# Kernel tuning notes

Hardware: AMD Instinct MI355X
Metric: run time of the kernel (lower is better)

The kernel has to match this reference:

```python
import jax, jax.numpy as jnp
import numpy as np

N_NODES = 50000
N_EDGES = 400000
DIMS = [128, 1024, 512, 256, 64, 1]  # ConvGraphNet layer widths


def setup_inputs() -> dict:
    key = jax.random.key(0)
    ks = jax.random.split(key, 2 + 2 * 5)
    inp = {}
    inp["x"] = jax.random.normal(ks[0], (N_NODES, DIMS[0]), dtype=jnp.float32)
    inp["edge_index"] = jax.random.randint(ks[1], (2, N_EDGES), 0, N_NODES, dtype=jnp.int32)
    for i in range(5):
        fan_in, fan_out = DIMS[i], DIMS[i + 1]
        scale = (1.0 / np.sqrt(fan_in)).astype(np.float32)
        inp[f"W{i+1}"] = jax.random.normal(ks[2 + 2 * i], (fan_in, fan_out), dtype=jnp.float32) * scale
        inp[f"b{i+1}"] = jax.random.normal(ks[3 + 2 * i], (fan_out,), dtype=jnp.float32) * 0.01
    return inp


def _gcn_forward(x, edge_index, params):
    # PyG GCNConv: add self-loops, symmetric deg^{-1/2} normalization,
    # h = x @ W, out[dst] += norm * h[src], + bias. ReLU after each layer.
    src, dst = edge_index[0], edge_index[1]
    loop = jnp.arange(N_NODES, dtype=src.dtype)
    src_f = jnp.concatenate([src, loop])  # [E + N]
    dst_f = jnp.concatenate([dst, loop])
    deg = jax.ops.segment_sum(jnp.ones_like(src_f, dtype=x.dtype), dst_f, num_segments=N_NODES)
    dinv = jnp.where(deg > 0, jax.lax.rsqrt(jnp.maximum(deg, 1e-12)), 0.0).astype(x.dtype)
    norm = (dinv[src_f] * dinv[dst_f])[:, None]  # [E + N, 1]
    for W, b in params:
        h = x @ W                      # [N, F_out] dense GEMM (small)
        msg = h[src_f] * norm          # gather + scale  [E+N, F_out]
        agg = jax.ops.segment_sum(msg, dst_f, num_segments=N_NODES)  # scatter-add
        x = jax.nn.relu(agg + b)
    return x


def reference(x, edge_index, W1, b1, W2, b2, W3, b3, W4, b4, W5, b5):
    params = [(W1, b1), (W2, b2), (W3, b3), (W4, b4), (W5, b5)]
    return _gcn_forward(x, edge_index, params)
```

## Files before the change

kernel.cpp:

```cpp
#include <hip/hip_runtime.h>
#include <hip/hip_bf16.h>

#define N_NODES_DIM0 128

typedef unsigned short u16;
typedef unsigned int u32;
typedef __attribute__((ext_vector_type(8))) short short8;
typedef __attribute__((ext_vector_type(4))) float f32x4;

__device__ __forceinline__ float bf2f(u16 h) { return __uint_as_float((u32)h << 16); }
__device__ __forceinline__ u16 f2bf(float f) {
    u32 u = __float_as_uint(f);
    u32 r = (u + 0x7FFFu + ((u >> 16) & 1u)) >> 16;
    return (u16)r;
}

__device__ __forceinline__ void gl2lds16(const u16* g, u16* lds_base) {
    __builtin_amdgcn_global_load_lds(
        (const __attribute__((address_space(1))) u32*)g,
        (__attribute__((address_space(3))) u32*)lds_base, 16, 0, 0);
}


__global__ void hist_kernel(const int* __restrict__ dst, int* __restrict__ cnt, int e) {
    int i = blockIdx.x * blockDim.x + threadIdx.x;
    if (i < e) atomicAdd(&cnt[dst[i]], 1);
}

__global__ void alloc_kernel(const int* __restrict__ cnt, int* __restrict__ row_start,
                             float* __restrict__ dinv, int* __restrict__ cursor, int n) {
    int i = blockIdx.x * blockDim.x + threadIdx.x;
    int lane = threadIdx.x & 63;
    int v = (i < n) ? cnt[i] : 0;
    int s = v;
#pragma unroll
    for (int off = 1; off < 64; off <<= 1) {
        int x = __shfl_up(s, off, 64);
        if (lane >= off) s += x;
    }
    int total = __shfl(s, 63, 64);
    int base = 0;
    if (lane == 0) base = atomicAdd(cursor, total);
    base = __shfl(base, 0, 64);
    if (i < n) {
        row_start[i] = base + s - v;
        dinv[i] = rsqrtf((float)v + 1.0f);
    }
}

__global__ void fill_kernel(const int* __restrict__ src, const int* __restrict__ dst,
                            int* __restrict__ row_start, int* __restrict__ csr_src, int e) {
    int i = blockIdx.x * blockDim.x + threadIdx.x;
    if (i < e) {
        int d = dst[i];
        int pos = atomicAdd(&row_start[d], 1);
        csr_src[pos] = src[i];
    }
}

__global__ __launch_bounds__(256) void prep_kernel(
    const float* __restrict__ W0, const float* __restrict__ W1,
    const float* __restrict__ W2, const float* __restrict__ W3, u16* __restrict__ Wt,
    const float* __restrict__ x, const float* __restrict__ dinv,
    u16* __restrict__ Y, int N) {
    int bid = blockIdx.x;
    if (bid < 784) {
        __shared__ float tile[32][33];
        const float* W; u16* out; int K, F, kb, nb;
        if (bid < 128)      { W = W0; out = Wt;          K = 128;  F = 1024; kb = bid & 3;  nb = bid >> 2; }
        else if (bid < 640) { int l = bid - 128; W = W1; out = Wt + 131072; K = 1024; F = 512; kb = l & 31; nb = l >> 5; }
        else if (bid < 768) { int l = bid - 640; W = W2; out = Wt + 655360; K = 512;  F = 256; kb = l & 15; nb = l >> 4; }
        else                { int l = bid - 768; W = W3; out = Wt + 786432; K = 256;  F = 64;  kb = l & 7;  nb = l >> 3; }
        int k0 = kb * 32, n0 = nb * 32;
        int tx = threadIdx.x & 31, ty = threadIdx.x >> 5;
#pragma unroll
        for (int i = 0; i < 4; ++i) {
            int k = ty + i * 8;
            tile[k][tx] = W[(size_t)(k0 + k) * F + n0 + tx];
        }
        __syncthreads();
#pragma unroll
        for (int i = 0; i < 4; ++i) {
            int n = ty + i * 8;
            out[(size_t)(n0 + n) * K + k0 + tx] = f2bf(tile[tx][n]);
        }
    } else {
        int gid = (bid - 784) * 256 + threadIdx.x;
        int node = gid >> 5;
        int c4 = (gid & 31) * 4;
        if (node >= N) return;
        float dv = dinv[node];
        float4 v = *reinterpret_cast<const float4*>(x + (size_t)node * 128 + c4);
        ushort4 r;
        r.x = f2bf(dv * v.x); r.y = f2bf(dv * v.y);
        r.z = f2bf(dv * v.z); r.w = f2bf(dv * v.w);
        *reinterpret_cast<ushort4*>(Y + (size_t)node * 128 + c4) = r;
    }
}

__device__ __forceinline__ void add8v(float* acc, short8 v) {
#pragma unroll
    for (int w = 0; w < 8; ++w) acc[w] += bf2f((u16)v[w]);
}
__device__ __forceinline__ void add16p(float* acc, const u16* p) {
    short8 a = *reinterpret_cast<const short8*>(p);
    short8 b = *reinterpret_cast<const short8*>(p + 8);
    add8v(acc, a); add8v(acc + 8, b);
}

__device__ __forceinline__ void gather_sum16(float* acc, const u16* __restrict__ base,
                                             const int* __restrict__ csr_src,
                                             int beg, int end, int stride, int ch) {
    int e = beg;
    int nfull = (end - beg) >> 3;
    if (nfull > 0) {
        int i0 = csr_src[e],     i1 = csr_src[e + 1], i2 = csr_src[e + 2], i3 = csr_src[e + 3];
        int i4 = csr_src[e + 4], i5 = csr_src[e + 5], i6 = csr_src[e + 6], i7 = csr_src[e + 7];
        for (int b = 0; b < nfull; ++b) {
            const u16* p0 = base + (size_t)i0 * stride + ch;
            const u16* p1 = base + (size_t)i1 * stride + ch;
            const u16* p2 = base + (size_t)i2 * stride + ch;
            const u16* p3 = base + (size_t)i3 * stride + ch;
            const u16* p4 = base + (size_t)i4 * stride + ch;
            const u16* p5 = base + (size_t)i5 * stride + ch;
            const u16* p6 = base + (size_t)i6 * stride + ch;
            const u16* p7 = base + (size_t)i7 * stride + ch;
            short8 a0 = *reinterpret_cast<const short8*>(p0), b0 = *reinterpret_cast<const short8*>(p0 + 8);
            short8 a1 = *reinterpret_cast<const short8*>(p1), b1 = *reinterpret_cast<const short8*>(p1 + 8);
            short8 a2 = *reinterpret_cast<const short8*>(p2), b2 = *reinterpret_cast<const short8*>(p2 + 8);
            short8 a3 = *reinterpret_cast<const short8*>(p3), b3 = *reinterpret_cast<const short8*>(p3 + 8);
            short8 a4 = *reinterpret_cast<const short8*>(p4), b4 = *reinterpret_cast<const short8*>(p4 + 8);
            short8 a5 = *reinterpret_cast<const short8*>(p5), b5 = *reinterpret_cast<const short8*>(p5 + 8);
            short8 a6 = *reinterpret_cast<const short8*>(p6), b6 = *reinterpret_cast<const short8*>(p6 + 8);
            short8 a7 = *reinterpret_cast<const short8*>(p7), b7 = *reinterpret_cast<const short8*>(p7 + 8);
            e += 8;
            int ep = (e + 8 <= end) ? e : beg;
            i0 = csr_src[ep];     i1 = csr_src[ep + 1]; i2 = csr_src[ep + 2]; i3 = csr_src[ep + 3];
            i4 = csr_src[ep + 4]; i5 = csr_src[ep + 5]; i6 = csr_src[ep + 6]; i7 = csr_src[ep + 7];
            __builtin_amdgcn_sched_barrier(0);
            add8v(acc, a0); add8v(acc + 8, b0);
            add8v(acc, a1); add8v(acc + 8, b1);
            add8v(acc, a2); add8v(acc + 8, b2);
            add8v(acc, a3); add8v(acc + 8, b3);
            add8v(acc, a4); add8v(acc + 8, b4);
            add8v(acc, a5); add8v(acc + 8, b5);
            add8v(acc, a6); add8v(acc + 8, b6);
            add8v(acc, a7); add8v(acc + 8, b7);
        }
    }
    for (; e + 4 <= end; e += 4) {
        const u16* p0 = base + (size_t)csr_src[e]     * stride + ch;
        const u16* p1 = base + (size_t)csr_src[e + 1] * stride + ch;
        const u16* p2 = base + (size_t)csr_src[e + 2] * stride + ch;
        const u16* p3 = base + (size_t)csr_src[e + 3] * stride + ch;
        short8 a0 = *reinterpret_cast<const short8*>(p0), b0 = *reinterpret_cast<const short8*>(p0 + 8);
        short8 a1 = *reinterpret_cast<const short8*>(p1), b1 = *reinterpret_cast<const short8*>(p1 + 8);
        short8 a2 = *reinterpret_cast<const short8*>(p2), b2 = *reinterpret_cast<const short8*>(p2 + 8);
        short8 a3 = *reinterpret_cast<const short8*>(p3), b3 = *reinterpret_cast<const short8*>(p3 + 8);
        __builtin_amdgcn_sched_barrier(0);
        add8v(acc, a0); add8v(acc + 8, b0);
        add8v(acc, a1); add8v(acc + 8, b1);
        add8v(acc, a2); add8v(acc + 8, b2);
        add8v(acc, a3); add8v(acc + 8, b3);
    }
    for (; e < end; ++e) {
        const u16* p = base + (size_t)csr_src[e] * stride + ch;
        short8 a = *reinterpret_cast<const short8*>(p), b = *reinterpret_cast<const short8*>(p + 8);
        add8v(acc, a); add8v(acc + 8, b);
    }
}

template <int TPB, int MODE>
__device__ __forceinline__ void agg_dev(
        int bid, int t, const int* __restrict__ row_end, const int* __restrict__ cnt,
        const int* __restrict__ csr_src, const u16* Gin, const float* __restrict__ dinv,
        const float* __restrict__ bias, u16* XO, int nodeBeg, int nodeEnd, int F, int lgG) {
    int gid = bid * TPB + t;
    int node = nodeBeg + (gid >> lgG);
    int ch = (gid & ((1 << lgG) - 1)) * 16;
    if (node >= nodeEnd) return;
    float acc[16] = {};
    add16p(acc, Gin + (size_t)node * F + ch);
    int end = row_end[node], beg = end - cnt[node];
    gather_sum16(acc, Gin, csr_src, beg, end, F, ch);
    float dv = dinv[node];
    short8 r0, r1;
#pragma unroll
    for (int w = 0; w < 8; ++w) {
        if (MODE == 0) {
            r0[w] = (short)f2bf(dv * acc[w]);
            r1[w] = (short)f2bf(dv * acc[8 + w]);
        } else {
            r0[w] = (short)f2bf(fmaxf(fmaf(dv, acc[w], bias[ch + w]), 0.f));
            r1[w] = (short)f2bf(fmaxf(fmaf(dv, acc[8 + w], bias[ch + 8 + w]), 0.f));
        }
    }
    *reinterpret_cast<short8*>(XO + (size_t)node * F + ch) = r0;
    *reinterpret_cast<short8*>(XO + (size_t)node * F + ch + 8) = r1;
}

template <int TPB, int MODE>
__global__ __launch_bounds__(TPB, 4) void agg_kernel(
        const int* __restrict__ row_end, const int* __restrict__ cnt,
        const int* __restrict__ csr_src, const u16* Gin, const float* __restrict__ dinv,
        const float* __restrict__ bias, u16* XO, int nodeBeg, int nodeEnd, int F, int lgG) {
    agg_dev<TPB, MODE>(blockIdx.x, threadIdx.x, row_end, cnt, csr_src, Gin, dinv, bias, XO,
                       nodeBeg, nodeEnd, F, lgG);
}

template <int BN, int TPB, int EPI>
__device__ __forceinline__ void gemm_dev(
    u16* As, u16* Bs, int bid, int t,
    const u16* X, const u16* __restrict__ Wt,
    const float* __restrict__ dinv, const float* __restrict__ bias,
    u16* Out, int rowBeg, int rowEnd, int N, int K, int F, int lgnx) {
    constexpr int BM = 128, BK = 64;
    constexpr int RA = (BM * 8) / TPB;
    constexpr int RB = (BN * 8) / TPB;
    constexpr int WAVES = TPB / 64;
    constexpr int WAVES_N = (BN >= 64) ? (BN / 64) : 1;
    constexpr int WAVES_M = WAVES / WAVES_N;
    constexpr int WM = BM / WAVES_M;
    constexpr int WN = BN / WAVES_N;
    constexpr int NI = WM / 16;
    constexpr int NJ = WN / 16;

    const int wave = t >> 6;
    const int lane = t & 63;
    const int m16 = lane & 15;
    const int quad = lane >> 4;

    const int wi = bid & ((8 << lgnx) - 1);
    const int g  = bid >> (3 + lgnx);
    const int rb = g * 8 + (wi & 7);
    const int cb = wi >> 3;
    const int row0 = rowBeg + rb * BM;
    const int col0 = cb * BN;
    if (row0 >= rowEnd) return;

    const int wm = (wave / WAVES_N) * WM;
    const int wn = (wave % WAVES_N) * WN;

    const u16* aSrc[RA];
    u16* aDst[RA];
#pragma unroll
    for (int rr = 0; rr < RA; ++rr) {
        int c = rr * TPB + t;
        int r = c >> 3;
        int q = (c ^ r) & 7;
        int grow = row0 + r;
        if (grow >= N) grow = 0;
        aSrc[rr] = X + (size_t)grow * K + q * 8;
        aDst[rr] = &As[(size_t)(rr * TPB + wave * 64) * 8];
    }
    const u16* bSrc[RB];
    u16* bDst[RB];
#pragma unroll
    for (int rr = 0; rr < RB; ++rr) {
        int c = rr * TPB + t;
        int r = c >> 3;
        int q = (c ^ r) & 7;
        bSrc[rr] = Wt + (size_t)(col0 + r) * K + q * 8;
        bDst[rr] = &Bs[(size_t)(rr * TPB + wave * 64) * 8];
    }

    u32 aOff[NI][2], bOff[NJ][2];
#pragma unroll
    for (int i = 0; i < NI; ++i)
#pragma unroll
        for (int h = 0; h < 2; ++h) {
            int row = wm + i * 16 + m16;
            int qg = h * 4 + quad;
            aOff[i][h] = (u32)(((row << 3) | ((qg ^ row) & 7)) * 16);
        }
#pragma unroll
    for (int j = 0; j < NJ; ++j)
#pragma unroll
        for (int h = 0; h < 2; ++h) {
            int row = wn + j * 16 + m16;
            int qg = h * 4 + quad;
            bOff[j][h] = (u32)(((row << 3) | ((qg ^ row) & 7)) * 16);
        }
    const char* AsB = reinterpret_cast<const char*>(As);
    const char* BsB = reinterpret_cast<const char*>(Bs);

    f32x4 acc[NI][NJ] = {};

    for (int k0 = 0; k0 < K; k0 += BK) {
#pragma unroll
        for (int rr = 0; rr < RA; ++rr) {
            gl2lds16(aSrc[rr], aDst[rr]);
            aSrc[rr] += BK;
        }
#pragma unroll
        for (int rr = 0; rr < RB; ++rr) {
            gl2lds16(bSrc[rr], bDst[rr]);
            bSrc[rr] += BK;
        }
        __syncthreads();

#pragma unroll
        for (int h = 0; h < 2; ++h) {
            short8 af[NI], bf[NJ];
#pragma unroll
            for (int i = 0; i < NI; ++i)
                af[i] = *reinterpret_cast<const short8*>(AsB + aOff[i][h]);
#pragma unroll
            for (int j = 0; j < NJ; ++j)
                bf[j] = *reinterpret_cast<const short8*>(BsB + bOff[j][h]);
#pragma unroll
            for (int i = 0; i < NI; ++i)
#pragma unroll
                for (int j = 0; j < NJ; ++j)
                    acc[i][j] = __builtin_amdgcn_mfma_f32_16x16x32_bf16(af[i], bf[j], acc[i][j], 0, 0, 0);
        }
        __syncthreads();
    }

#pragma unroll
    for (int i = 0; i < NI; ++i) {
#pragma unroll
        for (int r = 0; r < 4; ++r) {
            int grow = row0 + wm + i * 16 + quad * 4 + r;
            if (grow >= N) continue;
            float dv = (EPI == 0) ? dinv[grow] : 0.f;
#pragma unroll
            for (int j = 0; j < NJ; ++j) {
                int gcol = col0 + wn + j * 16 + m16;
                float v = acc[i][j][r];
                if (EPI == 0) v = dv * v;
                else          v = fmaxf(v + bias[gcol], 0.f);
                Out[(size_t)grow * F + gcol] = f2bf(v);
            }
        }
    }
}

template <int BN, int TPB, int EPI>
__global__ __launch_bounds__(TPB) void gemm_mfma_kernel(
    const u16* X, const u16* __restrict__ Wt,
    const float* __restrict__ dinv, const float* __restrict__ bias,
    u16* Out, int rowBeg, int rowEnd, int N, int K, int F, int lgnx) {
    __shared__ u16 As[128 * 64];
    __shared__ u16 Bs[BN * 64];
    gemm_dev<BN, TPB, EPI>(As, Bs, blockIdx.x, threadIdx.x, X, Wt, dinv, bias, Out,
                           rowBeg, rowEnd, N, K, F, lgnx);
}


__global__ __launch_bounds__(512) void fused_aggpre_gemm1_kernel(
        const int* __restrict__ row_end, const int* __restrict__ cnt,
        const int* __restrict__ csr_src, const u16* Y, const float* __restrict__ dinv,
        u16* Z, const u16* __restrict__ Wt0, const float* __restrict__ b0, u16* XA,
        int nG, int M0, int N) {
    __shared__ u16 As[128 * 64];
    __shared__ u16 Bs[256 * 64];
    int bid = blockIdx.x;
    if (bid < nG)
        gemm_dev<256, 512, 1>(As, Bs, bid, threadIdx.x, Z, Wt0, dinv, b0, XA,
                              0, M0, N, 128, 1024, 2);
    else
        agg_dev<512, 0>(bid - nG, threadIdx.x, row_end, cnt, csr_src, Y, dinv, nullptr, Z,
                        M0, N, 128, 3);
}

__global__ __launch_bounds__(512) void fused_agg2_gemm3_kernel(
        const int* __restrict__ row_end, const int* __restrict__ cnt,
        const int* __restrict__ csr_src, const u16* Gc512, const float* __restrict__ dinv,
        const float* __restrict__ b1, u16* XB, const u16* __restrict__ Wt2, u16* Gc256,
        int nG, int M0, int N) {
    __shared__ u16 As[128 * 64];
    __shared__ u16 Bs[256 * 64];
    int bid = blockIdx.x;
    if (bid < nG)
        gemm_dev<256, 512, 0>(As, Bs, bid, threadIdx.x, XB, Wt2, dinv, b1, Gc256,
                              0, M0, N, 512, 256, 0);
    else
        agg_dev<512, 1>(bid - nG, threadIdx.x, row_end, cnt, csr_src, Gc512, dinv, b1, XB,
                        M0, N, 512, 5);
}

__global__ __launch_bounds__(512) void fused_agg3_gemm4_kernel(
        const int* __restrict__ row_end, const int* __restrict__ cnt,
        const int* __restrict__ csr_src, const u16* Gc256, const float* __restrict__ dinv,
        const float* __restrict__ b2, u16* XAlow, const u16* __restrict__ Wt3,
        const float* __restrict__ b3, u16* Gc64, int nG, int M0, int N) {
    __shared__ u16 As[128 * 64];
    __shared__ u16 Bs[64 * 64];
    int bid = blockIdx.x;
    if (bid < nG)
        gemm_dev<64, 512, 0>(As, Bs, bid, threadIdx.x, XAlow, Wt3, dinv, b3, Gc64,
                             0, M0, N, 256, 64, 0);
    else
        agg_dev<512, 1>(bid - nG, threadIdx.x, row_end, cnt, csr_src, Gc256, dinv, b2, XAlow,
                        M0, N, 256, 4);
}

__global__ __launch_bounds__(256, 4) void agg_post_l5_kernel(
        const int* __restrict__ row_end, const int* __restrict__ cnt,
        const int* __restrict__ csr_src,
        const u16* __restrict__ Gc, const float* __restrict__ dinv,
        const float* __restrict__ b4, const float* __restrict__ W5,
        float* __restrict__ g5, int N) {
    int gid = blockIdx.x * blockDim.x + threadIdx.x;
    int node = gid >> 2;
    int ch = (gid & 3) * 16;
    if (node >= N) return;
    float acc[16] = {};
    add16p(acc, Gc + (size_t)node * 64 + ch);
    int end = row_end[node], beg = end - cnt[node];
    gather_sum16(acc, Gc, csr_src, beg, end, 64, ch);
    float dv = dinv[node];
    float dot = 0.f;
#pragma unroll
    for (int w = 0; w < 16; ++w) {
        float v = fmaxf(fmaf(dv, acc[w], b4[ch + w]), 0.f);
        dot = fmaf(v, W5[ch + w], dot);
    }
#pragma unroll
    for (int off = 2; off > 0; off >>= 1) dot += __shfl_down(dot, off, 4);
    if ((gid & 3) == 0) g5[node] = dv * dot;
}

__global__ void agg5_kernel(const int* __restrict__ row_end, const int* __restrict__ cnt,
                            const int* __restrict__ csr_src,
                            const float* __restrict__ g5, const float* __restrict__ dinv,
                            const float* __restrict__ b5, float* __restrict__ out, int N) {
    int i = blockIdx.x * blockDim.x + threadIdx.x;
    if (i >= N) return;
    float acc = g5[i];
    int end = row_end[i], e = end - cnt[i];
    for (; e + 4 <= end; e += 4) {
        float a = g5[csr_src[e]];
        float b = g5[csr_src[e + 1]];
        float c = g5[csr_src[e + 2]];
        float d = g5[csr_src[e + 3]];
        acc += (a + b) + (c + d);
    }
    for (; e < end; ++e) acc += g5[csr_src[e]];
    out[i] = fmaxf(fmaf(dinv[i], acc, b5[0]), 0.f);
}


static inline size_t align_up(size_t x) { return (x + 255) & ~(size_t)255; }
static inline int round_up8(int x) { return (x + 7) & ~7; }

extern "C" void kernel_launch(void* const* d_in, const int* in_sizes, int n_in,
                              void* d_out, int out_size, void* d_ws, size_t ws_size,
                              hipStream_t stream) {
    const float* x  = (const float*)d_in[0];
    const int*   ei = (const int*)d_in[1];
    const int E = in_sizes[1] / 2;
    const int N = in_sizes[0] / N_NODES_DIM0;
    const int* src = ei;
    const int* dst = ei + E;

    const float* W[5] = {(const float*)d_in[2], (const float*)d_in[4], (const float*)d_in[6],
                         (const float*)d_in[8], (const float*)d_in[10]};
    const float* B[5] = {(const float*)d_in[3], (const float*)d_in[5], (const float*)d_in[7],
                         (const float*)d_in[9], (const float*)d_in[11]};

    const int Ks[4] = {128, 1024, 512, 256};
    const int Fs[4] = {1024, 512, 256, 64};

    char* w = (char*)d_ws;
    size_t off = 0;
    float* dinv    = (float*)(w + off); off += align_up((size_t)N * 4);
    float* g5      = (float*)(w + off); off += align_up((size_t)N * 4);
    int*   cnt     = (int*)(w + off);   off += align_up((size_t)(N + 1) * 4);
    int*   rstart  = (int*)(w + off);   off += align_up((size_t)N * 4);
    int*   csr_src = (int*)(w + off);   off += align_up((size_t)E * 4);
    u16* WtBase = (u16*)(w + off);
    u16* Wt[4];
    {
        size_t cum = 0;
        for (int l = 0; l < 4; ++l) {
            Wt[l] = WtBase + cum;
            cum += (size_t)Ks[l] * Fs[l];
        }
        off += align_up(cum * 2);
    }
    char* REG = w + off;               off += align_up((size_t)N * 512 * 2);
    u16* Y  = (u16*)REG;
    u16* Z  = (u16*)(REG + align_up((size_t)N * 128 * 2));
    u16* Gc = (u16*)REG;
    u16* XA = (u16*)(w + off);         off += align_up((size_t)N * 1024 * 2);
    u16* XB = (u16*)(w + off);         off += align_up((size_t)N * 512 * 2);
    u16* Gc256 = XA + (size_t)N * 512;
    (void)ws_size;

    hipMemsetAsync(cnt, 0, (size_t)(N + 1) * 4, stream);
    hist_kernel<<<(E + 255) / 256, 256, 0, stream>>>(dst, cnt, E);
    alloc_kernel<<<(N + 255) / 256, 256, 0, stream>>>(cnt, rstart, dinv, &cnt[N], N);
    fill_kernel<<<(E + 255) / 256, 256, 0, stream>>>(src, dst, rstart, csr_src, E);

    {
        int scale_blocks = (N * 32 + 255) / 256;
        prep_kernel<<<784 + scale_blocks, 256, 0, stream>>>(
            W[0], W[1], W[2], W[3], WtBase, x, dinv, Y, N);
    }

    const int ny  = (N + 127) / 128;
    const int nyh = (ny + 1) / 2;
    const int M0  = nyh * 128;
    const int ny8  = round_up8(ny);
    const int ny8h = round_up8(nyh);
    const int ny8r = round_up8(ny - nyh);
    const int h1nodes = (N > M0) ? (N - M0) : 0;

    agg_kernel<256, 0><<<(M0 * 8 + 255) / 256, 256, 0, stream>>>(
        rstart, cnt, csr_src, Y, dinv, nullptr, Z, 0, M0 < N ? M0 : N, 128, 3);
    {
        int nG = ny8h * 4;
        int nA = (h1nodes * 8 + 511) / 512;
        fused_aggpre_gemm1_kernel<<<nG + nA, 512, 0, stream>>>(
            rstart, cnt, csr_src, Y, dinv, Z, Wt[0], B[0], XA, nG, M0, N);
    }
    if (ny > nyh)
        gemm_mfma_kernel<256, 512, 1><<<ny8r * 4, 512, 0, stream>>>(
            Z, Wt[0], dinv, B[0], XA, M0, N, N, 128, 1024, 2);

    gemm_mfma_kernel<256, 512, 0><<<ny8 * 2, 512, 0, stream>>>(
        XA, Wt[1], dinv, B[1], Gc, 0, N, N, 1024, 512, 1);

    agg_kernel<256, 1><<<(M0 * 32 + 255) / 256, 256, 0, stream>>>(
        rstart, cnt, csr_src, Gc, dinv, B[1], XB, 0, M0 < N ? M0 : N, 512, 5);
    {
        int nG = ny8h;
        int nA = (h1nodes * 32 + 511) / 512;
        fused_agg2_gemm3_kernel<<<nG + nA, 512, 0, stream>>>(
            rstart, cnt, csr_src, Gc, dinv, B[1], XB, Wt[2], Gc256, nG, M0, N);
    }
    if (ny > nyh)
        gemm_mfma_kernel<256, 512, 0><<<ny8r, 512, 0, stream>>>(
            XB, Wt[2], dinv, B[1], Gc256, M0, N, N, 512, 256, 0);

    agg_kernel<256, 1><<<(M0 * 16 + 255) / 256, 256, 0, stream>>>(
        rstart, cnt, csr_src, Gc256, dinv, B[2], XA, 0, M0 < N ? M0 : N, 256, 4);
    {
        int nG = ny8h;
        int nA = (h1nodes * 16 + 511) / 512;
        fused_agg3_gemm4_kernel<<<nG + nA, 512, 0, stream>>>(
            rstart, cnt, csr_src, Gc256, dinv, B[2], XA, Wt[3], B[3], Gc, nG, M0, N);
    }
    if (ny > nyh)
        gemm_mfma_kernel<64, 512, 0><<<ny8r, 512, 0, stream>>>(
            XA, Wt[3], dinv, B[3], Gc, M0, N, N, 256, 64, 0);

    agg_post_l5_kernel<<<(unsigned)(((long long)N * 4 + 255) / 256), 256, 0, stream>>>(
        rstart, cnt, csr_src, Gc, dinv, B[3], W[4], g5, N);

    agg5_kernel<<<(N + 255) / 256, 256, 0, stream>>>(rstart, cnt, csr_src, g5, dinv, B[4],
                                                     (float*)d_out, N);
}
```

Measured before the change: 442.8 us.

## Fuse prep kernels with CSR build and interleave agg/GEMM blocks in fused launches

The weight transpose now runs in the same launch as the degree histogram, and the x scaling runs in the same launch as the CSR fill. This drops one kernel launch and lets independent work share the device. In the three fused agg+GEMM kernels, block roles are no longer two contiguous ranges. The smaller role set is spread evenly among the larger one, so both kinds of work are dispatched together instead of one after the other. This aims to balance load across compute units, at the cost of extra index arithmetic and some mixing of LDS and register demand per CU.

```diff
diff --git a/kernel.cpp b/kernel.cpp
--- a/kernel.cpp
+++ b/kernel.cpp
@@ -22,9 +22,36 @@
 }
 
 
-__global__ void hist_kernel(const int* __restrict__ dst, int* __restrict__ cnt, int e) {
-    int i = blockIdx.x * blockDim.x + threadIdx.x;
-    if (i < e) atomicAdd(&cnt[dst[i]], 1);
+__global__ __launch_bounds__(256) void hist_wt_kernel(
+    const int* __restrict__ dst, int* __restrict__ cnt, int e, int histB,
+    const float* __restrict__ W0, const float* __restrict__ W1,
+    const float* __restrict__ W2, const float* __restrict__ W3, u16* __restrict__ Wt) {
+    __shared__ float tile[32][33];
+    int bid = blockIdx.x;
+    if (bid < histB) {
+        int i = bid * 256 + threadIdx.x;
+        if (i < e) atomicAdd(&cnt[dst[i]], 1);
+        return;
+    }
+    bid -= histB;
+    const float* W; u16* out; int K, F, kb, nb;
+    if (bid < 128)      { W = W0; out = Wt;          K = 128;  F = 1024; kb = bid & 3;  nb = bid >> 2; }
+    else if (bid < 640) { int l = bid - 128; W = W1; out = Wt + 131072; K = 1024; F = 512; kb = l & 31; nb = l >> 5; }
+    else if (bid < 768) { int l = bid - 640; W = W2; out = Wt + 655360; K = 512;  F = 256; kb = l & 15; nb = l >> 4; }
+    else                { int l = bid - 768; W = W3; out = Wt + 786432; K = 256;  F = 64;  kb = l & 7;  nb = l >> 3; }
+    int k0 = kb * 32, n0 = nb * 32;
+    int tx = threadIdx.x & 31, ty = threadIdx.x >> 5;
+#pragma unroll
+    for (int i = 0; i < 4; ++i) {
+        int k = ty + i * 8;
+        tile[k][tx] = W[(size_t)(k0 + k) * F + n0 + tx];
+    }
+    __syncthreads();
+#pragma unroll
+    for (int i = 0; i < 4; ++i) {
+        int n = ty + i * 8;
+        out[(size_t)(n0 + n) * K + k0 + tx] = f2bf(tile[tx][n]);
+    }
 }
 
 __global__ void alloc_kernel(const int* __restrict__ cnt, int* __restrict__ row_start,
@@ -48,54 +75,31 @@
     }
 }
 
-__global__ void fill_kernel(const int* __restrict__ src, const int* __restrict__ dst,
-                            int* __restrict__ row_start, int* __restrict__ csr_src, int e) {
-    int i = blockIdx.x * blockDim.x + threadIdx.x;
-    if (i < e) {
-        int d = dst[i];
-        int pos = atomicAdd(&row_start[d], 1);
-        csr_src[pos] = src[i];
-    }
-}
-
-__global__ __launch_bounds__(256) void prep_kernel(
-    const float* __restrict__ W0, const float* __restrict__ W1,
-    const float* __restrict__ W2, const float* __restrict__ W3, u16* __restrict__ Wt,
+__global__ __launch_bounds__(256) void fill_y_kernel(
+    const int* __restrict__ src, const int* __restrict__ dst,
+    int* __restrict__ row_start, int* __restrict__ csr_src, int e, int fillB,
     const float* __restrict__ x, const float* __restrict__ dinv,
     u16* __restrict__ Y, int N) {
     int bid = blockIdx.x;
-    if (bid < 784) {
-        __shared__ float tile[32][33];
-        const float* W; u16* out; int K, F, kb, nb;
-        if (bid < 128)      { W = W0; out = Wt;          K = 128;  F = 1024; kb = bid & 3;  nb = bid >> 2; }
-        else if (bid < 640) { int l = bid - 128; W = W1; out = Wt + 131072; K = 1024; F = 512; kb = l & 31; nb = l >> 5; }
-        else if (bid < 768) { int l = bid - 640; W = W2; out = Wt + 655360; K = 512;  F = 256; kb = l & 15; nb = l >> 4; }
-        else                { int l = bid - 768; W = W3; out = Wt + 786432; K = 256;  F = 64;  kb = l & 7;  nb = l >> 3; }
-        int k0 = kb * 32, n0 = nb * 32;
-        int tx = threadIdx.x & 31, ty = threadIdx.x >> 5;
-#pragma unroll
-        for (int i = 0; i < 4; ++i) {
-            int k = ty + i * 8;
-            tile[k][tx] = W[(size_t)(k0 + k) * F + n0 + tx];
-        }
-        __syncthreads();
-#pragma unroll
-        for (int i = 0; i < 4; ++i) {
-            int n = ty + i * 8;
-            out[(size_t)(n0 + n) * K + k0 + tx] = f2bf(tile[tx][n]);
-        }
-    } else {
-        int gid = (bid - 784) * 256 + threadIdx.x;
-        int node = gid >> 5;
-        int c4 = (gid & 31) * 4;
-        if (node >= N) return;
-        float dv = dinv[node];
-        float4 v = *reinterpret_cast<const float4*>(x + (size_t)node * 128 + c4);
-        ushort4 r;
-        r.x = f2bf(dv * v.x); r.y = f2bf(dv * v.y);
-        r.z = f2bf(dv * v.z); r.w = f2bf(dv * v.w);
-        *reinterpret_cast<ushort4*>(Y + (size_t)node * 128 + c4) = r;
-    }
+    if (bid < fillB) {
+        int i = bid * 256 + threadIdx.x;
+        if (i < e) {
+            int d = dst[i];
+            int pos = atomicAdd(&row_start[d], 1);
+            csr_src[pos] = src[i];
+        }
+        return;
+    }
+    int gid = (bid - fillB) * 256 + threadIdx.x;
+    int node = gid >> 5;
+    int c4 = (gid & 31) * 4;
+    if (node >= N) return;
+    float dv = dinv[node];
+    float4 v = *reinterpret_cast<const float4*>(x + (size_t)node * 128 + c4);
+    ushort4 r;
+    r.x = f2bf(dv * v.x); r.y = f2bf(dv * v.y);
+    r.z = f2bf(dv * v.z); r.w = f2bf(dv * v.w);
+    *reinterpret_cast<ushort4*>(Y + (size_t)node * 128 + c4) = r;
 }
 
 __device__ __forceinline__ void add8v(float* acc, short8 v) {
@@ -347,53 +351,67 @@
                            rowBeg, rowEnd, N, K, F, lgnx);
 }
 
+__device__ __forceinline__ bool pick_role(int bid, int nSmall, int k, int& sIdx, int& bIdx) {
+    int q = bid / k;
+    int r = bid - q * k;
+    if (r == 0 && q < nSmall) { sIdx = q; return true; }
+    bIdx = bid - ((q < nSmall) ? (q + (r ? 1 : 0)) : nSmall);
+    return false;
+}
 
 __global__ __launch_bounds__(512) void fused_aggpre_gemm1_kernel(
         const int* __restrict__ row_end, const int* __restrict__ cnt,
         const int* __restrict__ csr_src, const u16* Y, const float* __restrict__ dinv,
         u16* Z, const u16* __restrict__ Wt0, const float* __restrict__ b0, u16* XA,
-        int nG, int M0, int N) {
+        int nSmall, int k, int aggSmall, int M0, int N) {
     __shared__ u16 As[128 * 64];
     __shared__ u16 Bs[256 * 64];
-    int bid = blockIdx.x;
-    if (bid < nG)
-        gemm_dev<256, 512, 1>(As, Bs, bid, threadIdx.x, Z, Wt0, dinv, b0, XA,
+    int sIdx, bIdx;
+    bool isSmall = pick_role(blockIdx.x, nSmall, k, sIdx, bIdx);
+    int idx = isSmall ? sIdx : bIdx;
+    if (isSmall == (aggSmall != 0))
+        agg_dev<512, 0>(idx, threadIdx.x, row_end, cnt, csr_src, Y, dinv, nullptr, Z,
+                        M0, N, 128, 3);
+    else
+        gemm_dev<256, 512, 1>(As, Bs, idx, threadIdx.x, Z, Wt0, dinv, b0, XA,
                               0, M0, N, 128, 1024, 2);
-    else
-        agg_dev<512, 0>(bid - nG, threadIdx.x, row_end, cnt, csr_src, Y, dinv, nullptr, Z,
-                        M0, N, 128, 3);
 }
 
 __global__ __launch_bounds__(512) void fused_agg2_gemm3_kernel(
         const int* __restrict__ row_end, const int* __restrict__ cnt,
         const int* __restrict__ csr_src, const u16* Gc512, const float* __restrict__ dinv,
         const float* __restrict__ b1, u16* XB, const u16* __restrict__ Wt2, u16* Gc256,
-        int nG, int M0, int N) {
+        int nSmall, int k, int aggSmall, int M0, int N) {
     __shared__ u16 As[128 * 64];
     __shared__ u16 Bs[256 * 64];
-    int bid = blockIdx.x;
-    if (bid < nG)
-        gemm_dev<256, 512, 0>(As, Bs, bid, threadIdx.x, XB, Wt2, dinv, b1, Gc256,
+    int sIdx, bIdx;
+    bool isSmall = pick_role(blockIdx.x, nSmall, k, sIdx, bIdx);
+    int idx = isSmall ? sIdx : bIdx;
+    if (isSmall == (aggSmall != 0))
+        agg_dev<512, 1>(idx, threadIdx.x, row_end, cnt, csr_src, Gc512, dinv, b1, XB,
+                        M0, N, 512, 5);
+    else
+        gemm_dev<256, 512, 0>(As, Bs, idx, threadIdx.x, XB, Wt2, dinv, b1, Gc256,
                               0, M0, N, 512, 256, 0);
-    else
-        agg_dev<512, 1>(bid - nG, threadIdx.x, row_end, cnt, csr_src, Gc512, dinv, b1, XB,
-                        M0, N, 512, 5);
 }
 
 __global__ __launch_bounds__(512) void fused_agg3_gemm4_kernel(
         const int* __restrict__ row_end, const int* __restrict__ cnt,
         const int* __restrict__ csr_src, const u16* Gc256, const float* __restrict__ dinv,
         const float* __restrict__ b2, u16* XAlow, const u16* __restrict__ Wt3,
-        const float* __restrict__ b3, u16* Gc64, int nG, int M0, int N) {
+        const float* __restrict__ b3, u16* Gc64,
+        int nSmall, int k, int aggSmall, int M0, int N) {
     __shared__ u16 As[128 * 64];
     __shared__ u16 Bs[64 * 64];
-    int bid = blockIdx.x;
-    if (bid < nG)
-        gemm_dev<64, 512, 0>(As, Bs, bid, threadIdx.x, XAlow, Wt3, dinv, b3, Gc64,
+    int sIdx, bIdx;
+    bool isSmall = pick_role(blockIdx.x, nSmall, k, sIdx, bIdx);
+    int idx = isSmall ? sIdx : bIdx;
+    if (isSmall == (aggSmall != 0))
+        agg_dev<512, 1>(idx, threadIdx.x, row_end, cnt, csr_src, Gc256, dinv, b2, XAlow,
+                        M0, N, 256, 4);
+    else
+        gemm_dev<64, 512, 0>(As, Bs, idx, threadIdx.x, XAlow, Wt3, dinv, b3, Gc64,
                              0, M0, N, 256, 64, 0);
-    else
-        agg_dev<512, 1>(bid - nG, threadIdx.x, row_end, cnt, csr_src, Gc256, dinv, b2, XAlow,
-                        M0, N, 256, 4);
 }
 
 __global__ __launch_bounds__(256, 4) void agg_post_l5_kernel(
@@ -490,14 +508,17 @@
     (void)ws_size;
 
     hipMemsetAsync(cnt, 0, (size_t)(N + 1) * 4, stream);
-    hist_kernel<<<(E + 255) / 256, 256, 0, stream>>>(dst, cnt, E);
+    {
+        int histB = (E + 255) / 256;
+        hist_wt_kernel<<<histB + 784, 256, 0, stream>>>(dst, cnt, E, histB,
+                                                        W[0], W[1], W[2], W[3], WtBase);
+    }
     alloc_kernel<<<(N + 255) / 256, 256, 0, stream>>>(cnt, rstart, dinv, &cnt[N], N);
-    fill_kernel<<<(E + 255) / 256, 256, 0, stream>>>(src, dst, rstart, csr_src, E);
-
     {
-        int scale_blocks = (N * 32 + 255) / 256;
-        prep_kernel<<<784 + scale_blocks, 256, 0, stream>>>(
-            W[0], W[1], W[2], W[3], WtBase, x, dinv, Y, N);
+        int fillB = (E + 255) / 256;
+        int yB = (N * 32 + 255) / 256;
+        fill_y_kernel<<<fillB + yB, 256, 0, stream>>>(src, dst, rstart, csr_src, E, fillB,
+                                                      x, dinv, Y, N);
     }
 
     const int ny  = (N + 127) / 128;
@@ -508,13 +529,21 @@
     const int ny8r = round_up8(ny - nyh);
     const int h1nodes = (N > M0) ? (N - M0) : 0;
 
+    auto split = [](int nA, int nG, int& nSmall, int& k, int& aggSmall) {
+        if (nA <= nG) { nSmall = nA; aggSmall = 1; } else { nSmall = nG; aggSmall = 0; }
+        int T = nA + nG;
+        k = (nSmall > 0) ? (T / nSmall) : 1;
+        if (k < 1) k = 1;
+    };
+
     agg_kernel<256, 0><<<(M0 * 8 + 255) / 256, 256, 0, stream>>>(
         rstart, cnt, csr_src, Y, dinv, nullptr, Z, 0, M0 < N ? M0 : N, 128, 3);
     {
         int nG = ny8h * 4;
         int nA = (h1nodes * 8 + 511) / 512;
-        fused_aggpre_gemm1_kernel<<<nG + nA, 512, 0, stream>>>(
-            rstart, cnt, csr_src, Y, dinv, Z, Wt[0], B[0], XA, nG, M0, N);
+        int nS, k, aS; split(nA, nG, nS, k, aS);
+        fused_aggpre_gemm1_kernel<<<nA + nG, 512, 0, stream>>>(
+            rstart, cnt, csr_src, Y, dinv, Z, Wt[0], B[0], XA, nS, k, aS, M0, N);
     }
     if (ny > nyh)
         gemm_mfma_kernel<256, 512, 1><<<ny8r * 4, 512, 0, stream>>>(
@@ -528,8 +557,9 @@
     {
         int nG = ny8h;
         int nA = (h1nodes * 32 + 511) / 512;
-        fused_agg2_gemm3_kernel<<<nG + nA, 512, 0, stream>>>(
-            rstart, cnt, csr_src, Gc, dinv, B[1], XB, Wt[2], Gc256, nG, M0, N);
+        int nS, k, aS; split(nA, nG, nS, k, aS);
+        fused_agg2_gemm3_kernel<<<nA + nG, 512, 0, stream>>>(
+            rstart, cnt, csr_src, Gc, dinv, B[1], XB, Wt[2], Gc256, nS, k, aS, M0, N);
     }
     if (ny > nyh)
         gemm_mfma_kernel<256, 512, 0><<<ny8r, 512, 0, stream>>>(
@@ -540,8 +570,9 @@
     {
         int nG = ny8h;
         int nA = (h1nodes * 16 + 511) / 512;
-        fused_agg3_gemm4_kernel<<<nG + nA, 512, 0, stream>>>(
-            rstart, cnt, csr_src, Gc256, dinv, B[2], XA, Wt[3], B[3], Gc, nG, M0, N);
+        int nS, k, aS; split(nA, nG, nS, k, aS);
+        fused_agg3_gemm4_kernel<<<nA + nG, 512, 0, stream>>>(
+            rstart, cnt, csr_src, Gc256, dinv, B[2], XA, Wt[3], B[3], Gc, nS, k, aS, M0, N);
     }
     if (ny > nyh)
         gemm_mfma_kernel<64, 512, 0><<<ny8r, 512, 0, stream>>>(
```

Measured after the change: 469.8 us. 1.06x slower.
